# Kernel optimization log

Hardware: AMD Instinct MI355X
Metric: run time of the kernel (lower is better)

Reference implementation:

```python
import jax, jax.numpy as jnp
import numpy as np

B, S, H, E, K = 2, 1024, 1024, 8, 2
F = 4 * H


def setup_inputs() -> dict:
    key = jax.random.key(0)
    ks = jax.random.split(key, 8)
    std = 0.02
    return {
        "x": jax.random.normal(ks[0], (B, S, H), jnp.float32),
        "gate_w": jax.random.normal(ks[1], (E, H), jnp.float32) * (std / np.sqrt(H)),
        "gate_bias": jnp.zeros((E,), jnp.float32),
        "Wu": jax.random.normal(ks[2], (E, F, H), jnp.float32) * std,
        "bu": jnp.zeros((E, F), jnp.float32),
        "Wd": jax.random.normal(ks[3], (E, H, F), jnp.float32) * std,
        "bd": jnp.zeros((E, H), jnp.float32),
        "sWu": jax.random.normal(ks[4], (F, H), jnp.float32) * std,
        "sbu": jnp.zeros((F,), jnp.float32),
        "sWd": jax.random.normal(ks[5], (H, F), jnp.float32) * std,
        "sbd": jnp.zeros((H,), jnp.float32),
    }


def reference(x, gate_w, gate_bias, Wu, bu, Wd, bd, sWu, sbu, sWd, sbd):
    b, s, h = x.shape
    x_flat = x.reshape(-1, h)                      # [T, H]
    T = x_flat.shape[0]
    # Sigmoid gating + top-k (bias added before sigmoid, as in source)
    scores = jax.nn.sigmoid(x_flat @ gate_w.T + gate_bias)          # [T, E]
    top_scores, top_idx = jax.lax.top_k(scores, K)                  # [T, K]
    top_scores = top_scores / (top_scores.sum(-1, keepdims=True) + 1e-6)
    # Per-token per-expert combine weights (0 for non-selected experts)
    w = jnp.zeros((T, E), x.dtype).at[jnp.arange(T)[:, None], top_idx].add(top_scores)
    # Dense per-expert FFN over all tokens; masked out by w where not routed.
    h1 = jnp.einsum('th,efh->etf', x_flat, Wu) + bu[:, None, :]     # [E, T, F]
    a1 = jax.nn.gelu(h1, approximate=False)
    y = jnp.einsum('etf,ehf->eth', a1, Wd) + bd[:, None, :]         # [E, T, H]
    combined = jnp.einsum('te,eth->th', w, y)                       # [T, H]
    # Shared expert, scaled by 0.1
    sh = jax.nn.gelu(x_flat @ sWu.T + sbu, approximate=False)
    shared = (sh @ sWd.T + sbd) * 0.1
    return (combined + shared).reshape(b, s, h)
```

## Files before the change

### kernel.cpp

```cpp
#include <hip/hip_runtime.h>
#include <cstdint>
#include <cstddef>

#define T_TOK 2048
#define H_DIM 1024
#define E_NUM 8
#define F_DIM 4096
#define NG 9

typedef unsigned short ushort_t;
typedef __attribute__((ext_vector_type(8))) short bf16x8;
typedef __attribute__((ext_vector_type(4))) float f32x4;
typedef unsigned int u32;
typedef u32 __attribute__((address_space(3))) lds_u32;
typedef u32 __attribute__((address_space(1))) glob_u32;

constexpr size_t OFF_TTI = 0;
constexpr size_t OFF_TTW = 16u << 10;
constexpr size_t OFF_CNT = 32u << 10;
constexpr size_t OFF_OFFS = (32u << 10) + 256;
constexpr size_t OFF_RID = 64u << 10;
constexpr size_t OFF_WTS = 96u << 10;
constexpr size_t OFF_XBF = 1u << 20;
constexpr size_t OFF_WUB = 8u << 20;
constexpr size_t OFF_WDB = 80u << 20;
constexpr size_t OFF_A   = 152u << 20;
constexpr size_t OFF_Y   = 200u << 20;
constexpr size_t Y_SPLIT_STRIDE = (size_t)T_TOK * 3 * H_DIM;

__device__ __forceinline__ ushort_t f2bf(float f) {
  union { float f; unsigned u; } v; v.f = f;
  unsigned r = v.u + 0x7FFFu + ((v.u >> 16) & 1u);
  return (ushort_t)(r >> 16);
}

__device__ __forceinline__ float bf2f(ushort_t b) {
  union { unsigned u; float f; } v; v.u = ((unsigned)b) << 16;
  return v.f;
}

__device__ __forceinline__ float gelu_fast(float v) {
  const float x = v * 0.70710678118654752f;
  const float xa = fabsf(x);
  const float t = __builtin_amdgcn_rcpf(fmaf(0.3275911f, xa, 1.0f));
  float p = fmaf(1.061405429f, t, -1.453152027f);
  p = fmaf(p, t, 1.421413741f);
  p = fmaf(p, t, -0.284496736f);
  p = fmaf(p, t, 0.254829592f);
  p = p * t;
  const float e = __expf(-xa * xa);
  float erfa = fmaf(-p, e, 1.0f);
  erfa = copysignf(erfa, x);
  return 0.5f * v * (1.0f + erfa);
}

__device__ __forceinline__ void gll16(const ushort_t* g, ushort_t* l) {
  __builtin_amdgcn_global_load_lds((glob_u32*)(g), (lds_u32*)(l), 16, 0, 0);
}

#define VMCNT0_BARRIER do { \
  asm volatile("s_waitcnt vmcnt(0)" ::: "memory"); \
  __builtin_amdgcn_s_barrier(); \
} while (0)

__global__ __launch_bounds__(256) void route_k(const float* __restrict__ x,
                                               const float* __restrict__ gw,
                                               const float* __restrict__ gb,
                                               int* __restrict__ tt_idx,
                                               float* __restrict__ tt_w) {
  const int lane = threadIdx.x & 63;
  const int wid = threadIdx.x >> 6;
  const int t = blockIdx.x * 4 + wid;
  if (t >= T_TOK) return;
  const float* xr = x + (size_t)t * H_DIM;
  float acc[8] = {0.f, 0.f, 0.f, 0.f, 0.f, 0.f, 0.f, 0.f};
  for (int i = 0; i < H_DIM; i += 64) {
    const int k = i + lane;
    const float xv = xr[k];
#pragma unroll
    for (int e = 0; e < 8; ++e) acc[e] = fmaf(xv, gw[e * H_DIM + k], acc[e]);
  }
#pragma unroll
  for (int e = 0; e < 8; ++e) {
    float v = acc[e];
#pragma unroll
    for (int s = 32; s; s >>= 1) v += __shfl_xor(v, s, 64);
    acc[e] = v;
  }
  if (lane == 0) {
    float sc[8];
#pragma unroll
    for (int e = 0; e < 8; ++e) sc[e] = 1.0f / (1.0f + expf(-(acc[e] + gb[e])));
    int i0 = 0;
#pragma unroll
    for (int e = 1; e < 8; ++e) if (sc[e] > sc[i0]) i0 = e;
    int i1 = (i0 == 0) ? 1 : 0;
#pragma unroll
    for (int e = 0; e < 8; ++e) if (e != i0 && sc[e] > sc[i1]) i1 = e;
    const float d = sc[i0] + sc[i1] + 1e-6f;
    tt_idx[2 * t] = i0;
    tt_idx[2 * t + 1] = i1;
    tt_w[2 * t] = sc[i0] / d;
    tt_w[2 * t + 1] = sc[i1] / d;
  }
}

__global__ __launch_bounds__(256) void build_k(const int* __restrict__ tt_idx,
                                               const float* __restrict__ tt_w,
                                               int* __restrict__ counts,
                                               int* __restrict__ offs,
                                               int* __restrict__ rid,
                                               float* __restrict__ wts) {
  __shared__ int cnt[NG];
  __shared__ int cur[NG];
  const int tid = threadIdx.x;
  if (tid < NG) cnt[tid] = 0;
  __syncthreads();
  for (int p = tid; p < 2 * T_TOK; p += 256) atomicAdd(&cnt[tt_idx[p]], 1);
  __syncthreads();
  if (tid == 0) {
    int run = 0;
    for (int e = 0; e < E_NUM; ++e) {
      offs[e] = run;
      counts[e] = cnt[e];
      cur[e] = run;
      run += cnt[e];
    }
    offs[E_NUM] = 2 * T_TOK;
    counts[E_NUM] = T_TOK;
    cur[E_NUM] = 2 * T_TOK;
  }
  __syncthreads();
  for (int p = tid; p < 2 * T_TOK; p += 256) {
    const int e = tt_idx[p];
    const int pos = atomicAdd(&cur[e], 1);
    rid[pos] = ((p >> 1) << 2) | (p & 1);
    wts[pos] = tt_w[p];
  }
  for (int p = tid; p < T_TOK; p += 256) {
    rid[2 * T_TOK + p] = (p << 2) | 2;
    wts[2 * T_TOK + p] = 0.1f;
  }
}

__global__ __launch_bounds__(256) void convert_k(const float* __restrict__ Wu,
                                                 const float* __restrict__ sWu,
                                                 const float* __restrict__ Wd,
                                                 const float* __restrict__ sWd,
                                                 const float* __restrict__ x,
                                                 ushort_t* __restrict__ Wub,
                                                 ushort_t* __restrict__ Wdb,
                                                 ushort_t* __restrict__ Xbf) {
  const long WE = (long)NG * F_DIM * H_DIM;
  const long W8 = (long)8 * F_DIM * H_DIM;
  const long XE = (long)T_TOK * H_DIM;
  const long total = (2 * WE + XE) / 8;
  for (long i = blockIdx.x * 256L + threadIdx.x; i < total; i += (long)gridDim.x * 256L) {
    const long base = i * 8;
    const float* src;
    ushort_t* dst;
    if (base < WE) {
      const long o = base;
      src = (o < W8) ? (Wu + o) : (sWu + (o - W8));
      dst = Wub + o;
    } else if (base < 2 * WE) {
      const long o = base - WE;
      src = (o < W8) ? (Wd + o) : (sWd + (o - W8));
      dst = Wdb + o;
    } else {
      const long o = base - 2 * WE;
      src = x + o;
      dst = Xbf + o;
    }
    const float4 v0 = *(const float4*)src;
    const float4 v1 = *(const float4*)(src + 4);
    bf16x8 r;
    r[0] = (short)f2bf(v0.x); r[1] = (short)f2bf(v0.y);
    r[2] = (short)f2bf(v0.z); r[3] = (short)f2bf(v0.w);
    r[4] = (short)f2bf(v1.x); r[5] = (short)f2bf(v1.y);
    r[6] = (short)f2bf(v1.z); r[7] = (short)f2bf(v1.w);
    *(bf16x8*)dst = r;
  }
}

#define STAGE_T(A_, B_, k0_) do { \
  _Pragma("unroll") \
  for (int i_ = 0; i_ < 4; ++i_) { \
    gll16(pA[i_] + (k0_), &(A_)[(wid * 4 + i_) * 512]); \
    gll16(pB[i_] + (k0_), &(B_)[(wid * 4 + i_) * 512]); \
  } \
} while (0)

#define COMPUTE_T(A_, B_) do { \
  _Pragma("unroll") \
  for (int ks_ = 0; ks_ < 2; ++ks_) { \
    const int cc_ = ks_ * 4 + hi; \
    bf16x8 af_[4], bv_[4]; \
    _Pragma("unroll") \
    for (int m_ = 0; m_ < 4; ++m_) { \
      const int r_ = wr + m_ * 16 + fr; \
      af_[m_] = *(const bf16x8*)&(A_)[r_ * 64 + ((cc_ ^ (r_ & 7)) << 3)]; \
    } \
    _Pragma("unroll") \
    for (int n_ = 0; n_ < 4; ++n_) { \
      const int r_ = wc + n_ * 16 + fr; \
      bv_[n_] = *(const bf16x8*)&(B_)[r_ * 64 + ((cc_ ^ (r_ & 7)) << 3)]; \
    } \
    _Pragma("unroll") \
    for (int m_ = 0; m_ < 4; ++m_) \
      _Pragma("unroll") \
      for (int n_ = 0; n_ < 4; ++n_) \
        acc[m_][n_] = __builtin_amdgcn_mfma_f32_16x16x32_bf16(af_[m_], bv_[n_], acc[m_][n_], 0, 0, 0); \
  } \
} while (0)

__global__ __launch_bounds__(256) void up_gemm(const ushort_t* __restrict__ Xbf,
                                               const ushort_t* __restrict__ Wub,
                                               const int* __restrict__ counts,
                                               const int* __restrict__ offs,
                                               const int* __restrict__ rid,
                                               const float* __restrict__ wts,
                                               const float* __restrict__ bu,
                                               const float* __restrict__ sbu,
                                               ushort_t* __restrict__ Aout) {
  const int g = blockIdx.y >> 4;
  const int mt = blockIdx.y & 15;
  const int rows = counts[g];
  if (mt * 128 >= rows) return;
  const int off = offs[g];
  const int n0 = blockIdx.x * 128;

  __shared__ ushort_t lds[4][128 * 64];

  const int tid = threadIdx.x;
  const int lane = tid & 63;
  const int wid = tid >> 6;
  const int sr = lane >> 3;
  const int swz = ((lane & 7) ^ sr) << 3;

  const ushort_t* Wg = Wub + (size_t)g * F_DIM * H_DIM;
  const ushort_t* pA[4];
  const ushort_t* pB[4];
#pragma unroll
  for (int i = 0; i < 4; ++i) {
    const int rA = (wid * 4 + i) * 8 + sr;
    int ig = mt * 128 + rA;
    if (ig >= rows) ig = rows - 1;
    pA[i] = Xbf + (size_t)(rid[off + ig] >> 2) * H_DIM + swz;
    pB[i] = Wg + (size_t)(n0 + rA) * H_DIM + swz;
  }

  f32x4 acc[4][4];
#pragma unroll
  for (int m = 0; m < 4; ++m)
#pragma unroll
    for (int n = 0; n < 4; ++n) acc[m][n] = (f32x4){0.f, 0.f, 0.f, 0.f};

  const int wr = (wid >> 1) * 64;
  const int wc = (wid & 1) * 64;
  const int fr = lane & 15;
  const int hi = lane >> 4;

  STAGE_T(lds[0], lds[1], 0);
  VMCNT0_BARRIER;
#pragma unroll 1
  for (int kt = 0; kt < 16; kt += 2) {
    STAGE_T(lds[2], lds[3], (kt + 1) * 64);
    COMPUTE_T(lds[0], lds[1]);
    VMCNT0_BARRIER;
    if (kt + 2 < 16) STAGE_T(lds[0], lds[1], (kt + 2) * 64);
    COMPUTE_T(lds[2], lds[3]);
    VMCNT0_BARRIER;
  }

  const float* bug = (g < E_NUM) ? (bu + (size_t)g * F_DIM) : sbu;
#pragma unroll
  for (int m = 0; m < 4; ++m) {
#pragma unroll
    for (int q = 0; q < 4; ++q) {
      const int r = wr + m * 16 + hi * 4 + q;
      const int ig = mt * 128 + r;
      if (ig < rows) {
        const float wrow = wts[off + ig];
        const size_t rowbase = (size_t)(off + ig) * F_DIM + n0;
#pragma unroll
        for (int n = 0; n < 4; ++n) {
          const int c = wc + n * 16 + fr;
          const float v = acc[m][n][q] + bug[n0 + c];
          Aout[rowbase + c] = f2bf(gelu_fast(v) * wrow);
        }
      }
    }
  }
}

__global__ __launch_bounds__(256) void down_gemm(const ushort_t* __restrict__ Ain,
                                                 const ushort_t* __restrict__ Wdb,
                                                 const int* __restrict__ counts,
                                                 const int* __restrict__ offs,
                                                 const int* __restrict__ rid,
                                                 ushort_t* __restrict__ Ybf) {
  const int g = blockIdx.y >> 4;
  const int mt = blockIdx.y & 15;
  const int rows = counts[g];
  if (mt * 128 >= rows) return;
  const int off = offs[g];
  const int n0 = blockIdx.x * 128;
  const int kbase = blockIdx.z * 2048;
  ushort_t* Ys = Ybf + (size_t)blockIdx.z * Y_SPLIT_STRIDE;

  __shared__ ushort_t lds[4][128 * 64];

  const int tid = threadIdx.x;
  const int lane = tid & 63;
  const int wid = tid >> 6;
  const int sr = lane >> 3;
  const int swz = ((lane & 7) ^ sr) << 3;

  const ushort_t* Wg = Wdb + (size_t)g * H_DIM * F_DIM;
  const ushort_t* pA[4];
  const ushort_t* pB[4];
#pragma unroll
  for (int i = 0; i < 4; ++i) {
    const int rA = (wid * 4 + i) * 8 + sr;
    pA[i] = Ain + (size_t)(off + mt * 128 + rA) * F_DIM + kbase + swz;
    pB[i] = Wg + (size_t)(n0 + rA) * F_DIM + kbase + swz;
  }

  f32x4 acc[4][4];
#pragma unroll
  for (int m = 0; m < 4; ++m)
#pragma unroll
    for (int n = 0; n < 4; ++n) acc[m][n] = (f32x4){0.f, 0.f, 0.f, 0.f};

  const int wr = (wid >> 1) * 64;
  const int wc = (wid & 1) * 64;
  const int fr = lane & 15;
  const int hi = lane >> 4;

  STAGE_T(lds[0], lds[1], 0);
  VMCNT0_BARRIER;
#pragma unroll 1
  for (int kt = 0; kt < 32; kt += 2) {
    STAGE_T(lds[2], lds[3], (kt + 1) * 64);
    COMPUTE_T(lds[0], lds[1]);
    VMCNT0_BARRIER;
    if (kt + 2 < 32) STAGE_T(lds[0], lds[1], (kt + 2) * 64);
    COMPUTE_T(lds[2], lds[3]);
    VMCNT0_BARRIER;
  }

#pragma unroll
  for (int m = 0; m < 4; ++m) {
#pragma unroll
    for (int q = 0; q < 4; ++q) {
      const int r = wr + m * 16 + hi * 4 + q;
      const int ig = mt * 128 + r;
      if (ig < rows) {
        const int rv = rid[off + ig];
        ushort_t* yrow = Ys + ((size_t)(rv >> 2) * 3 + (rv & 3)) * H_DIM + n0;
#pragma unroll
        for (int n = 0; n < 4; ++n) {
          const int c = wc + n * 16 + fr;
          yrow[c] = f2bf(acc[m][n][q]);
        }
      }
    }
  }
}

__global__ __launch_bounds__(256) void combine_k(const ushort_t* __restrict__ Ybf,
                                                 const int* __restrict__ tt_idx,
                                                 const float* __restrict__ tt_w,
                                                 const float* __restrict__ bd,
                                                 const float* __restrict__ sbd,
                                                 float* __restrict__ out) {
  const int t = blockIdx.x;
  const int h = threadIdx.x * 4;
  const int e0 = tt_idx[2 * t];
  const int e1 = tt_idx[2 * t + 1];
  const float w0 = tt_w[2 * t];
  const float w1 = tt_w[2 * t + 1];
  float s[4] = {0.f, 0.f, 0.f, 0.f};
#pragma unroll
  for (int sp = 0; sp < 2; ++sp) {
#pragma unroll
    for (int sl = 0; sl < 3; ++sl) {
      const ushort_t* yp = Ybf + sp * Y_SPLIT_STRIDE + ((size_t)t * 3 + sl) * H_DIM + h;
      const ushort4 v = *(const ushort4*)yp;
      s[0] += bf2f(v.x); s[1] += bf2f(v.y); s[2] += bf2f(v.z); s[3] += bf2f(v.w);
    }
  }
  const float4 b0 = *(const float4*)(bd + (size_t)e0 * H_DIM + h);
  const float4 b1 = *(const float4*)(bd + (size_t)e1 * H_DIM + h);
  const float4 bs = *(const float4*)(sbd + h);
  float4 o;
  o.x = s[0] + w0 * b0.x + w1 * b1.x + 0.1f * bs.x;
  o.y = s[1] + w0 * b0.y + w1 * b1.y + 0.1f * bs.y;
  o.z = s[2] + w0 * b0.z + w1 * b1.z + 0.1f * bs.z;
  o.w = s[3] + w0 * b0.w + w1 * b1.w + 0.1f * bs.w;
  *(float4*)(out + (size_t)t * H_DIM + h) = o;
}

extern "C" void kernel_launch(void* const* d_in, const int* in_sizes, int n_in,
                              void* d_out, int out_size, void* d_ws, size_t ws_size,
                              hipStream_t stream) {
  (void)in_sizes; (void)n_in; (void)out_size; (void)ws_size;
  const float* x = (const float*)d_in[0];
  const float* gate_w = (const float*)d_in[1];
  const float* gate_b = (const float*)d_in[2];
  const float* Wu = (const float*)d_in[3];
  const float* bu = (const float*)d_in[4];
  const float* Wd = (const float*)d_in[5];
  const float* bd = (const float*)d_in[6];
  const float* sWu = (const float*)d_in[7];
  const float* sbu = (const float*)d_in[8];
  const float* sWd = (const float*)d_in[9];
  const float* sbd = (const float*)d_in[10];
  float* out = (float*)d_out;

  char* ws = (char*)d_ws;
  int* tt_idx = (int*)(ws + OFF_TTI);
  float* tt_w = (float*)(ws + OFF_TTW);
  int* counts = (int*)(ws + OFF_CNT);
  int* offs = (int*)(ws + OFF_OFFS);
  int* rid = (int*)(ws + OFF_RID);
  float* wts = (float*)(ws + OFF_WTS);
  ushort_t* Xbf = (ushort_t*)(ws + OFF_XBF);
  ushort_t* Wub = (ushort_t*)(ws + OFF_WUB);
  ushort_t* Wdb = (ushort_t*)(ws + OFF_WDB);
  ushort_t* A = (ushort_t*)(ws + OFF_A);
  ushort_t* Y = (ushort_t*)(ws + OFF_Y);

  hipLaunchKernelGGL(route_k, dim3(T_TOK / 4), dim3(256), 0, stream,
                     x, gate_w, gate_b, tt_idx, tt_w);
  hipLaunchKernelGGL(build_k, dim3(1), dim3(256), 0, stream,
                     tt_idx, tt_w, counts, offs, rid, wts);
  hipLaunchKernelGGL(convert_k, dim3(4096), dim3(256), 0, stream,
                     Wu, sWu, Wd, sWd, x, Wub, Wdb, Xbf);
  hipLaunchKernelGGL(up_gemm, dim3(F_DIM / 128, NG * 16), dim3(256), 0, stream,
                     Xbf, Wub, counts, offs, rid, wts, bu, sbu, A);
  hipLaunchKernelGGL(down_gemm, dim3(H_DIM / 128, NG * 16, 2), dim3(256), 0, stream,
                     A, Wdb, counts, offs, rid, Y);
  hipLaunchKernelGGL(combine_k, dim3(T_TOK), dim3(256), 0, stream,
                     Y, tt_idx, tt_w, bd, sbd, out);
}
```

Before: 548.1 us.

## Fuse fp32-to-bf16 weight conversion into GEMM B-tile loading

Drops the separate pass that converts every expert weight matrix to bf16. The up and down GEMMs now load fp32 weight tiles straight into registers, pack them with v_cvt_pk_bf16_f32 and write the swizzled result into LDS, while the activation tiles still use direct global-to-LDS loads. This removes a full read and write of about 300 MB of weights in a separate kernel. In exchange, each GEMM block re-reads fp32 weights (twice the bytes) for every M-tile, and the pipeline adds register pressure plus an lgkmcnt wait at each barrier.

```diff
diff --git a/kernel.cpp b/kernel.cpp
--- a/kernel.cpp
+++ b/kernel.cpp
@@ -22,10 +22,8 @@
 constexpr size_t OFF_RID = 64u << 10;
 constexpr size_t OFF_WTS = 96u << 10;
 constexpr size_t OFF_XBF = 1u << 20;
-constexpr size_t OFF_WUB = 8u << 20;
-constexpr size_t OFF_WDB = 80u << 20;
-constexpr size_t OFF_A   = 152u << 20;
-constexpr size_t OFF_Y   = 200u << 20;
+constexpr size_t OFF_A   = 8u << 20;
+constexpr size_t OFF_Y   = 56u << 20;
 constexpr size_t Y_SPLIT_STRIDE = (size_t)T_TOK * 3 * H_DIM;
 
 __device__ __forceinline__ ushort_t f2bf(float f) {
@@ -37,6 +35,12 @@
 __device__ __forceinline__ float bf2f(ushort_t b) {
   union { unsigned u; float f; } v; v.u = ((unsigned)b) << 16;
   return v.f;
+}
+
+__device__ __forceinline__ u32 cvtpk_bf16(float a, float b) {
+  u32 r;
+  asm("v_cvt_pk_bf16_f32 %0, %1, %2" : "=v"(r) : "v"(a), "v"(b));
+  return r;
 }
 
 __device__ __forceinline__ float gelu_fast(float v) {
@@ -58,8 +62,8 @@
   __builtin_amdgcn_global_load_lds((glob_u32*)(g), (lds_u32*)(l), 16, 0, 0);
 }
 
-#define VMCNT0_BARRIER do { \
-  asm volatile("s_waitcnt vmcnt(0)" ::: "memory"); \
+#define WAITBAR do { \
+  asm volatile("s_waitcnt vmcnt(0) lgkmcnt(0)" ::: "memory"); \
   __builtin_amdgcn_s_barrier(); \
 } while (0)
 
@@ -143,51 +147,41 @@
   }
 }
 
-__global__ __launch_bounds__(256) void convert_k(const float* __restrict__ Wu,
-                                                 const float* __restrict__ sWu,
-                                                 const float* __restrict__ Wd,
-                                                 const float* __restrict__ sWd,
-                                                 const float* __restrict__ x,
-                                                 ushort_t* __restrict__ Wub,
-                                                 ushort_t* __restrict__ Wdb,
+__global__ __launch_bounds__(256) void convert_x(const float* __restrict__ x,
                                                  ushort_t* __restrict__ Xbf) {
-  const long WE = (long)NG * F_DIM * H_DIM;
-  const long W8 = (long)8 * F_DIM * H_DIM;
-  const long XE = (long)T_TOK * H_DIM;
-  const long total = (2 * WE + XE) / 8;
-  for (long i = blockIdx.x * 256L + threadIdx.x; i < total; i += (long)gridDim.x * 256L) {
-    const long base = i * 8;
-    const float* src;
-    ushort_t* dst;
-    if (base < WE) {
-      const long o = base;
-      src = (o < W8) ? (Wu + o) : (sWu + (o - W8));
-      dst = Wub + o;
-    } else if (base < 2 * WE) {
-      const long o = base - WE;
-      src = (o < W8) ? (Wd + o) : (sWd + (o - W8));
-      dst = Wdb + o;
-    } else {
-      const long o = base - 2 * WE;
-      src = x + o;
-      dst = Xbf + o;
-    }
-    const float4 v0 = *(const float4*)src;
-    const float4 v1 = *(const float4*)(src + 4);
-    bf16x8 r;
-    r[0] = (short)f2bf(v0.x); r[1] = (short)f2bf(v0.y);
-    r[2] = (short)f2bf(v0.z); r[3] = (short)f2bf(v0.w);
-    r[4] = (short)f2bf(v1.x); r[5] = (short)f2bf(v1.y);
-    r[6] = (short)f2bf(v1.z); r[7] = (short)f2bf(v1.w);
-    *(bf16x8*)dst = r;
-  }
-}
-
-#define STAGE_T(A_, B_, k0_) do { \
+  const long i = ((long)blockIdx.x * 256 + threadIdx.x) * 8;
+  const float4 v0 = *(const float4*)(x + i);
+  const float4 v1 = *(const float4*)(x + i + 4);
+  bf16x8 r;
+  r[0] = (short)f2bf(v0.x); r[1] = (short)f2bf(v0.y);
+  r[2] = (short)f2bf(v0.z); r[3] = (short)f2bf(v0.w);
+  r[4] = (short)f2bf(v1.x); r[5] = (short)f2bf(v1.y);
+  r[6] = (short)f2bf(v1.z); r[7] = (short)f2bf(v1.w);
+  *(bf16x8*)(Xbf + i) = r;
+}
+
+#define STAGEA(A_, k0_) do { \
   _Pragma("unroll") \
-  for (int i_ = 0; i_ < 4; ++i_) { \
+  for (int i_ = 0; i_ < 4; ++i_) \
     gll16(pA[i_] + (k0_), &(A_)[(wid * 4 + i_) * 512]); \
-    gll16(pB[i_] + (k0_), &(B_)[(wid * 4 + i_) * 512]); \
+} while (0)
+
+#define BLOADM(k0_) do { \
+  _Pragma("unroll") \
+  for (int j_ = 0; j_ < 8; ++j_) \
+    breg[j_] = *((const f32x4*)(pBf + (k0_)) + j_); \
+} while (0)
+
+#define CVTW(B_) do { \
+  _Pragma("unroll") \
+  for (int j_ = 0; j_ < 4; ++j_) { \
+    const int c_ = bhalf * 4 + j_; \
+    uint4 w_; \
+    w_.x = cvtpk_bf16(breg[2 * j_][0], breg[2 * j_][1]); \
+    w_.y = cvtpk_bf16(breg[2 * j_][2], breg[2 * j_][3]); \
+    w_.z = cvtpk_bf16(breg[2 * j_ + 1][0], breg[2 * j_ + 1][1]); \
+    w_.w = cvtpk_bf16(breg[2 * j_ + 1][2], breg[2 * j_ + 1][3]); \
+    *(uint4*)&(B_)[brow * 64 + ((c_ ^ (brow & 7)) << 3)] = w_; \
   } \
 } while (0)
 
@@ -214,8 +208,31 @@
   } \
 } while (0)
 
+#define GEMM_PIPELINE(NT_) do { \
+  STAGEA(lds[0], 0); \
+  BLOADM(0); \
+  CVTW(lds[1]); \
+  WAITBAR; \
+  _Pragma("unroll 1") \
+  for (int kt = 0; kt < (NT_); kt += 2) { \
+    BLOADM((kt + 1) * 64); \
+    STAGEA(lds[2], (kt + 1) * 64); \
+    COMPUTE_T(lds[0], lds[1]); \
+    CVTW(lds[3]); \
+    WAITBAR; \
+    if (kt + 2 < (NT_)) { \
+      BLOADM((kt + 2) * 64); \
+      STAGEA(lds[0], (kt + 2) * 64); \
+    } \
+    COMPUTE_T(lds[2], lds[3]); \
+    if (kt + 2 < (NT_)) CVTW(lds[1]); \
+    WAITBAR; \
+  } \
+} while (0)
+
 __global__ __launch_bounds__(256) void up_gemm(const ushort_t* __restrict__ Xbf,
-                                               const ushort_t* __restrict__ Wub,
+                                               const float* __restrict__ Wuf,
+                                               const float* __restrict__ sWuf,
                                                const int* __restrict__ counts,
                                                const int* __restrict__ offs,
                                                const int* __restrict__ rid,
@@ -237,18 +254,20 @@
   const int wid = tid >> 6;
   const int sr = lane >> 3;
   const int swz = ((lane & 7) ^ sr) << 3;
-
-  const ushort_t* Wg = Wub + (size_t)g * F_DIM * H_DIM;
+  const int brow = tid >> 1;
+  const int bhalf = tid & 1;
+
   const ushort_t* pA[4];
-  const ushort_t* pB[4];
 #pragma unroll
   for (int i = 0; i < 4; ++i) {
     const int rA = (wid * 4 + i) * 8 + sr;
     int ig = mt * 128 + rA;
     if (ig >= rows) ig = rows - 1;
     pA[i] = Xbf + (size_t)(rid[off + ig] >> 2) * H_DIM + swz;
-    pB[i] = Wg + (size_t)(n0 + rA) * H_DIM + swz;
-  }
+  }
+  const float* Wgf = (g < E_NUM) ? (Wuf + (size_t)g * F_DIM * H_DIM) : sWuf;
+  const float* pBf = Wgf + (size_t)(n0 + brow) * H_DIM + bhalf * 32;
+  f32x4 breg[8];
 
   f32x4 acc[4][4];
 #pragma unroll
@@ -261,17 +280,7 @@
   const int fr = lane & 15;
   const int hi = lane >> 4;
 
-  STAGE_T(lds[0], lds[1], 0);
-  VMCNT0_BARRIER;
-#pragma unroll 1
-  for (int kt = 0; kt < 16; kt += 2) {
-    STAGE_T(lds[2], lds[3], (kt + 1) * 64);
-    COMPUTE_T(lds[0], lds[1]);
-    VMCNT0_BARRIER;
-    if (kt + 2 < 16) STAGE_T(lds[0], lds[1], (kt + 2) * 64);
-    COMPUTE_T(lds[2], lds[3]);
-    VMCNT0_BARRIER;
-  }
+  GEMM_PIPELINE(16);
 
   const float* bug = (g < E_NUM) ? (bu + (size_t)g * F_DIM) : sbu;
 #pragma unroll
@@ -295,7 +304,8 @@
 }
 
 __global__ __launch_bounds__(256) void down_gemm(const ushort_t* __restrict__ Ain,
-                                                 const ushort_t* __restrict__ Wdb,
+                                                 const float* __restrict__ Wdf,
+                                                 const float* __restrict__ sWdf,
                                                  const int* __restrict__ counts,
                                                  const int* __restrict__ offs,
                                                  const int* __restrict__ rid,
@@ -316,16 +326,18 @@
   const int wid = tid >> 6;
   const int sr = lane >> 3;
   const int swz = ((lane & 7) ^ sr) << 3;
-
-  const ushort_t* Wg = Wdb + (size_t)g * H_DIM * F_DIM;
+  const int brow = tid >> 1;
+  const int bhalf = tid & 1;
+
   const ushort_t* pA[4];
-  const ushort_t* pB[4];
 #pragma unroll
   for (int i = 0; i < 4; ++i) {
     const int rA = (wid * 4 + i) * 8 + sr;
     pA[i] = Ain + (size_t)(off + mt * 128 + rA) * F_DIM + kbase + swz;
-    pB[i] = Wg + (size_t)(n0 + rA) * F_DIM + kbase + swz;
-  }
+  }
+  const float* Wgf = (g < E_NUM) ? (Wdf + (size_t)g * H_DIM * F_DIM) : sWdf;
+  const float* pBf = Wgf + (size_t)(n0 + brow) * F_DIM + kbase + bhalf * 32;
+  f32x4 breg[8];
 
   f32x4 acc[4][4];
 #pragma unroll
@@ -338,17 +350,7 @@
   const int fr = lane & 15;
   const int hi = lane >> 4;
 
-  STAGE_T(lds[0], lds[1], 0);
-  VMCNT0_BARRIER;
-#pragma unroll 1
-  for (int kt = 0; kt < 32; kt += 2) {
-    STAGE_T(lds[2], lds[3], (kt + 1) * 64);
-    COMPUTE_T(lds[0], lds[1]);
-    VMCNT0_BARRIER;
-    if (kt + 2 < 32) STAGE_T(lds[0], lds[1], (kt + 2) * 64);
-    COMPUTE_T(lds[2], lds[3]);
-    VMCNT0_BARRIER;
-  }
+  GEMM_PIPELINE(32);
 
 #pragma unroll
   for (int m = 0; m < 4; ++m) {
@@ -427,8 +429,6 @@
   int* rid = (int*)(ws + OFF_RID);
   float* wts = (float*)(ws + OFF_WTS);
   ushort_t* Xbf = (ushort_t*)(ws + OFF_XBF);
-  ushort_t* Wub = (ushort_t*)(ws + OFF_WUB);
-  ushort_t* Wdb = (ushort_t*)(ws + OFF_WDB);
   ushort_t* A = (ushort_t*)(ws + OFF_A);
   ushort_t* Y = (ushort_t*)(ws + OFF_Y);
 
@@ -436,12 +436,12 @@
                      x, gate_w, gate_b, tt_idx, tt_w);
   hipLaunchKernelGGL(build_k, dim3(1), dim3(256), 0, stream,
                      tt_idx, tt_w, counts, offs, rid, wts);
-  hipLaunchKernelGGL(convert_k, dim3(4096), dim3(256), 0, stream,
-                     Wu, sWu, Wd, sWd, x, Wub, Wdb, Xbf);
+  hipLaunchKernelGGL(convert_x, dim3(1024), dim3(256), 0, stream,
+                     x, Xbf);
   hipLaunchKernelGGL(up_gemm, dim3(F_DIM / 128, NG * 16), dim3(256), 0, stream,
-                     Xbf, Wub, counts, offs, rid, wts, bu, sbu, A);
+                     Xbf, Wu, sWu, counts, offs, rid, wts, bu, sbu, A);
   hipLaunchKernelGGL(down_gemm, dim3(H_DIM / 128, NG * 16, 2), dim3(256), 0, stream,
-                     A, Wdb, counts, offs, rid, Y);
+                     A, Wd, sWd, counts, offs, rid, Y);
   hipLaunchKernelGGL(combine_k, dim3(T_TOK), dim3(256), 0, stream,
                      Y, tt_idx, tt_w, bd, sbd, out);
 }
```

Result: slower. 627.1 us (+14.4%).
